# Kernel tuning notes

Measured on AMD Instinct MI355X. Metric: run time of the kernel, lower is better.

Reference implementation:

```python
import jax, jax.numpy as jnp
import numpy as np
import math

MAX_LEN = 65536
NUM_HEADS = 16
HEAD_DIM = 64
K_MAX = 64
LOCAL_WINDOW = 512
LOG_N = math.ceil(math.log2(MAX_LEN + 1))   # 17
LEAF_START = 2 ** LOG_N                      # segment-tree leaf offset


def cover_set(pos):
    """O(log n) segment-tree nodes covering prefix [0..pos-1], each with leaf-depth."""
    if pos <= 0:
        return []
    l, r = LEAF_START, LEAF_START + min(pos, MAX_LEN)
    out = []
    while l < r:
        if l & 1:
            out.append((l, LOG_N - int(math.floor(math.log2(l)))))
            l += 1
        if r & 1:
            r -= 1
            out.append((r, LOG_N - int(math.floor(math.log2(r)))))
        l >>= 1
        r >>= 1
    return out


def node_content(v_tokens, node_idx, depth):
    """Content of a FULL subtree node under the concat/pairwise-mean gated merge.
    Equals: concat tokens while K<=k_max, then (left+right)/2 elementwise, which
    collapses to a strided mean over chunks of size L//K_MAX. Returns (H, K, D)."""
    L = 1 << depth
    a = (node_idx << depth) - LEAF_START          # first token covered by node
    chunk = v_tokens[a:a + L]                     # (L, H, D), static slice
    if L <= K_MAX:
        f = chunk                                 # (L, H, D)
    else:
        f = chunk.reshape(L // K_MAX, K_MAX, NUM_HEADS, HEAD_DIM).mean(0)  # (K_MAX,H,D)
    return jnp.transpose(f, (1, 0, 2))            # (H, K, D)


def setup_inputs() -> dict:
    key = jax.random.key(0)
    k1, k2, k3 = jax.random.split(key, 3)
    v_tokens = jax.random.normal(k1, (50000, NUM_HEADS, HEAD_DIM), jnp.float32)
    q_new = jax.random.normal(k2, (1, NUM_HEADS, HEAD_DIM), jnp.float32)
    depth_proj_w = jax.random.normal(k3, (LOG_N + 1, HEAD_DIM, HEAD_DIM), jnp.float32) * 0.02
    depth_temp = jnp.linspace(0.5, 4.0, LOG_N + 1).astype(jnp.float32)
    return {"v_tokens": v_tokens, "q_new": q_new, "depth_proj_w": depth_proj_w,
            "depth_temp": depth_temp, "n_tokens": 50000}


def reference(v_tokens, q_new, depth_proj_w, depth_temp, n_tokens):
    pos = int(n_tokens)
    q = q_new[0]                                   # (H, D)
    inv_sqrt_d = 1.0 / math.sqrt(HEAD_DIM)

    # --- local window attention over last min(pos, W) tokens (chronological) ---
    n_local = min(pos, LOCAL_WINDOW)
    v_local = v_tokens[pos - n_local:pos]          # (W, H, D)
    s = jnp.einsum('hd,khd->hk', q, v_local) * inv_sqrt_d
    w = jax.nn.softmax(s, axis=-1)
    local_out = jnp.einsum('hk,khd->hd', w, v_local)   # (H, D)

    # --- multi-depth causal tree attention over the O(log n) cover set ---
    node_outs = []
    for node_idx, depth in cover_set(pos):
        f = node_content(v_tokens, node_idx, depth)    # (H, K, D)
        q_depth = q + q @ depth_proj_w[depth].T        # depth-specific query delta
        scale = 1.0 / ((jax.nn.softplus(depth_temp[depth]) + 1e-6) * math.sqrt(HEAD_DIM))
        s = jnp.einsum('hd,hkd->hk', q_depth, f) * scale
        w = jnp.einsum('hk,hkd->hd', jax.nn.softmax(s, axis=-1), f)
        node_outs.append(w)
    if node_outs:
        tree_out = jnp.stack(node_outs, axis=0).mean(0)
    else:
        tree_out = jnp.zeros_like(local_out)

    return (local_out + tree_out)[None]            # (1, H, D)
```

## Files before the change

### kernel.cpp

```cpp
#include <hip/hip_runtime.h>
#include <math.h>

#define NUM_HEADS   16
#define HEAD_DIM    64
#define KMAXN       64
#define LOCAL_WIN   512
#define LOG_N       17
#define LEAF_START  131072
#define MAX_LEN_TOK 65536
#define ROW         1024
#define SLICE       65536
#define MAXN        34

struct K1Args {
    int nNodes;
    int a[MAXN];
    int cpb[MAXN];
    int C[MAXN];
    int CB[MAXN];
    int K[MAXN];
    int off[MAXN];
    int bbase[MAXN];
};

struct K2Args {
    int nNodes;
    int K[MAXN];
    int C[MAXN];
    int CB[MAXN];
    int off[MAXN];
    int depth[MAXN];
};

__device__ __forceinline__ void f4add(float4& a, const float4& b) {
    a.x += b.x; a.y += b.y; a.z += b.z; a.w += b.w;
}

__global__ __launch_bounds__(256) void k1_reduce(const float* __restrict__ v,
                                                 float* __restrict__ ws,
                                                 K1Args A) {
    int b = blockIdx.x;
    int node = 0;
    for (int i = 1; i < A.nNodes; ++i)
        if (b >= A.bbase[i]) node = i;
    int lb  = b - A.bbase[node];
    int CB  = A.CB[node];
    int kg  = lb / CB;
    int cb  = lb - kg * CB;
    int k0  = kg * 16;
    int K   = A.K[node];
    int RK  = K - k0; if (RK > 16) RK = 16;
    int c0  = cb * A.cpb[node];
    int c1  = c0 + A.cpb[node];
    int C   = A.C[node];
    if (c1 > C) c1 = C;

    int j = threadIdx.x;

    float4 acc[16];
    #pragma unroll
    for (int r = 0; r < 16; ++r) acc[r] = make_float4(0.f, 0.f, 0.f, 0.f);

    if (RK == 16) {
        for (int c = c0; c < c1; ++c) {
            const float* p = v + (long)(A.a[node] + c * 64 + k0) * ROW + j * 4;
            float4 x[16];
            #pragma unroll
            for (int r = 0; r < 16; ++r) x[r] = *(const float4*)(p + r * ROW);
            #pragma unroll
            for (int r = 0; r < 16; ++r) f4add(acc[r], x[r]);
        }
    } else {
        for (int c = c0; c < c1; ++c) {
            const float* p = v + (long)(A.a[node] + c * 64 + k0) * ROW + j * 4;
            for (int r = 0; r < RK; ++r) f4add(acc[r], *(const float4*)(p + r * ROW));
        }
    }

    float* wp = ws + (long)A.off[node] + (long)cb * SLICE + (long)k0 * ROW + j * 4;
    for (int r = 0; r < RK; ++r)
        *(float4*)(wp + (long)r * ROW) = acc[r];
}

__global__ __launch_bounds__(256) void k1b_finalize(const float* __restrict__ ws_in,
                                                    float* __restrict__ f,
                                                    K2Args A) {
    int node = blockIdx.y;
    int k    = blockIdx.x;
    if (k >= A.K[node]) return;
    int CB = A.CB[node];
    const float* pf = ws_in + (long)A.off[node] + (long)k * ROW + threadIdx.x * 4;
    float4 a0 = make_float4(0.f,0.f,0.f,0.f);
    float4 a1 = a0, a2 = a0, a3 = a0;
    int cb = 0;
    for (; cb + 4 <= CB; cb += 4) {
        f4add(a0, *(const float4*)(pf + (long)cb * SLICE));
        f4add(a1, *(const float4*)(pf + (long)(cb+1) * SLICE));
        f4add(a2, *(const float4*)(pf + (long)(cb+2) * SLICE));
        f4add(a3, *(const float4*)(pf + (long)(cb+3) * SLICE));
    }
    for (; cb < CB; ++cb) f4add(a0, *(const float4*)(pf + (long)cb * SLICE));
    f4add(a0,a1); f4add(a2,a3); f4add(a0,a2);
    float invC = 1.0f / (float)A.C[node];
    a0.x*=invC; a0.y*=invC; a0.z*=invC; a0.w*=invC;
    *(float4*)(f + ((long)node * 64 + k) * ROW + threadIdx.x * 4) = a0;
}

__global__ __launch_bounds__(256) void k2_node_attn(const float* __restrict__ f,
                                                    const float* __restrict__ q,
                                                    const float* __restrict__ W,
                                                    const float* __restrict__ temp,
                                                    float* __restrict__ node_out,
                                                    K2Args A) {
    int h    = blockIdx.x;
    int node = blockIdx.y;
    int lane = threadIdx.x & 63;
    int w    = threadIdx.x >> 6;
    int K    = A.K[node];
    int dep  = A.depth[node];
    const float* pf = f + (long)node * SLICE + h * 64;

    __shared__ float qs[64], qds[64], sv[64], ps[64];
    __shared__ float red[4][64];

    if (threadIdx.x < 64) qs[lane] = q[h * 64 + lane];
    __syncthreads();

    float qp = 0.f;
    const float* Wr = W + ((long)dep * 64 + lane) * 64;
    #pragma unroll
    for (int e = w * 16; e < w * 16 + 16; ++e) qp += qs[e] * Wr[e];
    red[w][lane] = qp;
    __syncthreads();
    if (w == 0) qds[lane] = qs[lane] + red[0][lane] + red[1][lane] + red[2][lane] + red[3][lane];
    __syncthreads();
    float qd = qds[lane];

    float sp    = log1pf(expf(temp[dep]));
    float scale = 1.0f / ((sp + 1e-6f) * 8.0f);

    for (int k = w; k < K; k += 4) {
        float p = qd * pf[(long)k * ROW + lane];
        #pragma unroll
        for (int m = 1; m < 64; m <<= 1) p += __shfl_xor(p, m, 64);
        if (lane == 0) sv[k] = p * scale;
    }
    __syncthreads();

    if (w == 0) {
        float s  = (lane < K) ? sv[lane] : -1e30f;
        float mx = s;
        #pragma unroll
        for (int m = 1; m < 64; m <<= 1) mx = fmaxf(mx, __shfl_xor(mx, m, 64));
        float e = (lane < K) ? expf(s - mx) : 0.f;
        float S = e;
        #pragma unroll
        for (int m = 1; m < 64; m <<= 1) S += __shfl_xor(S, m, 64);
        ps[lane] = e / S;
    }
    __syncthreads();

    float o = 0.f;
    for (int k = w; k < K; k += 4) o += ps[k] * pf[(long)k * ROW + lane];
    red[w][lane] = o;
    __syncthreads();
    if (w == 0)
        node_out[node * ROW + h * 64 + lane] =
            red[0][lane] + red[1][lane] + red[2][lane] + red[3][lane];
}

__global__ __launch_bounds__(512) void k3_local(const float* __restrict__ v,
                                                const float* __restrict__ q,
                                                const float* __restrict__ node_out,
                                                int nNodes, int pos,
                                                float* __restrict__ out) {
    int h    = blockIdx.x;
    int tid  = threadIdx.x;
    int lane = tid & 63;
    int w    = tid >> 6;
    int nloc = pos < LOCAL_WIN ? pos : LOCAL_WIN;
    int t0   = pos - nloc;

    __shared__ float qs[64];
    __shared__ float sc[LOCAL_WIN];
    __shared__ float red[8][64];
    __shared__ float wred[16];
    __shared__ float mS[2];

    if (tid < 64) qs[tid] = q[h * 64 + tid];
    __syncthreads();

    float s = -1e30f;
    if (tid < nloc) {
        const float* vr = v + (long)(t0 + tid) * ROW + h * 64;
        float acc = 0.f;
        #pragma unroll 8
        for (int d = 0; d < 64; ++d) acc += qs[d] * vr[d];
        s = acc * 0.125f;
    }
    float mx = s;
    #pragma unroll
    for (int m = 1; m < 64; m <<= 1) mx = fmaxf(mx, __shfl_xor(mx, m, 64));
    if (lane == 0) wred[w] = mx;
    __syncthreads();
    if (tid == 0) {
        float m2 = wred[0];
        for (int i = 1; i < 8; ++i) m2 = fmaxf(m2, wred[i]);
        mS[0] = m2;
    }
    __syncthreads();
    float m = mS[0];

    float e = (tid < nloc) ? expf(s - m) : 0.f;
    sc[tid] = e;
    float su = e;
    #pragma unroll
    for (int mm = 1; mm < 64; mm <<= 1) su += __shfl_xor(su, mm, 64);
    if (lane == 0) wred[8 + w] = su;
    __syncthreads();
    if (tid == 0) {
        float S2 = 0.f;
        for (int i = 0; i < 8; ++i) S2 += wred[8 + i];
        mS[1] = S2;
    }
    __syncthreads();
    float S = mS[1];

    float acc = 0.f;
    {
        const float* vb = v + (long)t0 * ROW + h * 64 + lane;
        int tb = w * 64;
        #pragma unroll 4
        for (int i = 0; i < 64; ++i) {
            int t = tb + i;
            if (t < nloc) acc += sc[t] * vb[(long)t * ROW];
        }
    }
    red[w][lane] = acc;
    __syncthreads();

    if (w == 0) {
        float tot = 0.f;
        #pragma unroll
        for (int i = 0; i < 8; ++i) tot += red[i][lane];
        tot = (nloc > 0) ? tot / S : 0.f;
        float tr = 0.f;
        for (int n = 0; n < nNodes; ++n) tr += node_out[n * ROW + h * 64 + lane];
        if (nNodes > 0) tr /= (float)nNodes;
        out[h * 64 + lane] = tot + tr;
    }
}

static int floor_log2_host(unsigned x) { int r = 0; while (x >>= 1) ++r; return r; }

extern "C" void kernel_launch(void* const* d_in, const int* in_sizes, int n_in,
                              void* d_out, int out_size, void* d_ws, size_t ws_size,
                              hipStream_t stream) {
    const float* v    = (const float*)d_in[0];
    const float* q    = (const float*)d_in[1];
    const float* W    = (const float*)d_in[2];
    const float* temp = (const float*)d_in[3];
    float* out        = (float*)d_out;
    float* ws         = (float*)d_ws;

    int pos = in_sizes[0] / ROW;

    int n_nodes = 0;
    int nv[MAXN], nd[MAXN];
    if (pos > 0) {
        long l = LEAF_START;
        long r = LEAF_START + (pos < MAX_LEN_TOK ? pos : MAX_LEN_TOK);
        while (l < r) {
            if (l & 1) { nv[n_nodes] = (int)l; nd[n_nodes] = LOG_N - floor_log2_host((unsigned)l); ++n_nodes; ++l; }
            if (r & 1) { --r; nv[n_nodes] = (int)r; nd[n_nodes] = LOG_N - floor_log2_host((unsigned)r); ++n_nodes; }
            l >>= 1; r >>= 1;
        }
    }

    int cpb_choice = 1024;
    for (int cand : {8, 16, 32, 64, 128, 256, 512, 1024}) {
        long tot_cb = 0;
        for (int i = 0; i < n_nodes; ++i) {
            int L = 1 << nd[i];
            int C = (L > KMAXN) ? L / KMAXN : 1;
            tot_cb += (C + cand - 1) / cand;
        }
        long need = ((tot_cb + n_nodes) * (long)SLICE + (long)n_nodes * ROW) * 4;
        if (need <= (long)ws_size) { cpb_choice = cand; break; }
    }

    K1Args A1{}; K2Args A2{};
    A1.nNodes = n_nodes; A2.nNodes = n_nodes;
    int off = 0, bb = 0;
    for (int i = 0; i < n_nodes; ++i) {
        int depth = nd[i];
        int L = 1 << depth;
        int a = (nv[i] << depth) - LEAF_START;
        int K = (L < KMAXN) ? L : KMAXN;
        int C = (L > KMAXN) ? L / KMAXN : 1;
        int CB = (C + cpb_choice - 1) / cpb_choice;
        int cpb = (C + CB - 1) / CB;
        int kgc = (K + 15) / 16;
        A1.a[i] = a;   A1.cpb[i] = cpb; A1.C[i] = C; A1.CB[i] = CB; A1.K[i] = K;
        A1.off[i] = off; A1.bbase[i] = bb;
        A2.K[i] = K;   A2.C[i] = C;    A2.CB[i] = CB;
        A2.off[i] = off; A2.depth[i] = depth;
        off += CB * SLICE;
        bb  += kgc * CB;
    }
    float* f_buf     = ws + (long)off;
    float* node_outp = f_buf + (long)n_nodes * SLICE;

    if (n_nodes > 0) {
        hipLaunchKernelGGL(k1_reduce, dim3(bb), dim3(256), 0, stream, v, ws, A1);
        hipLaunchKernelGGL(k1b_finalize, dim3(64, n_nodes), dim3(256), 0, stream,
                           ws, f_buf, A2);
        hipLaunchKernelGGL(k2_node_attn, dim3(NUM_HEADS, n_nodes), dim3(256), 0, stream,
                           f_buf, q, W, temp, node_outp, A2);
    }
    hipLaunchKernelGGL(k3_local, dim3(NUM_HEADS), dim3(512), 0, stream,
                       v, q, node_outp, n_nodes, pos, out);
}
```

Measured before the change: 351.5 us.

## Split reduce blocks into 4-row groups with nontemporal loads and occupancy hint

Each k1_reduce block now covers 4 of the K rows instead of 16, so four times as many blocks are launched and each thread holds four accumulators instead of sixteen. The block index order changes so that row groups vary fastest within a chunk range. The inner loop is unrolled over two chunks and reads through nontemporal loads, and launch_bounds asks for 4 blocks per SM. The aim is more parallelism and higher occupancy on this streaming read, at the cost of more blocks and less memory-level parallelism per thread.

```diff
diff --git a/kernel.cpp b/kernel.cpp
--- a/kernel.cpp
+++ b/kernel.cpp
@@ -12,6 +12,12 @@
 #define SLICE       65536
 #define MAXN        34
 
+typedef float vf4 __attribute__((ext_vector_type(4)));
+
+__device__ __forceinline__ vf4 ntload(const float* p) {
+    return __builtin_nontemporal_load((const vf4*)p);
+}
+
 struct K1Args {
     int nNodes;
     int a[MAXN];
@@ -36,50 +42,66 @@
     a.x += b.x; a.y += b.y; a.z += b.z; a.w += b.w;
 }
 
-__global__ __launch_bounds__(256) void k1_reduce(const float* __restrict__ v,
-                                                 float* __restrict__ ws,
-                                                 K1Args A) {
+__global__ __launch_bounds__(256, 4) void k1_reduce(const float* __restrict__ v,
+                                                    float* __restrict__ ws,
+                                                    K1Args A) {
     int b = blockIdx.x;
     int node = 0;
     for (int i = 1; i < A.nNodes; ++i)
         if (b >= A.bbase[i]) node = i;
     int lb  = b - A.bbase[node];
-    int CB  = A.CB[node];
-    int kg  = lb / CB;
-    int cb  = lb - kg * CB;
-    int k0  = kg * 16;
     int K   = A.K[node];
-    int RK  = K - k0; if (RK > 16) RK = 16;
+    int kgc = (K + 3) >> 2;
+    int cb  = lb / kgc;
+    int kg  = lb - cb * kgc;
+    int k0  = kg * 4;
+    int RK  = K - k0; if (RK > 4) RK = 4;
     int c0  = cb * A.cpb[node];
     int c1  = c0 + A.cpb[node];
     int C   = A.C[node];
     if (c1 > C) c1 = C;
 
-    int j = threadIdx.x;
-
-    float4 acc[16];
-    #pragma unroll
-    for (int r = 0; r < 16; ++r) acc[r] = make_float4(0.f, 0.f, 0.f, 0.f);
-
-    if (RK == 16) {
-        for (int c = c0; c < c1; ++c) {
-            const float* p = v + (long)(A.a[node] + c * 64 + k0) * ROW + j * 4;
-            float4 x[16];
-            #pragma unroll
-            for (int r = 0; r < 16; ++r) x[r] = *(const float4*)(p + r * ROW);
-            #pragma unroll
-            for (int r = 0; r < 16; ++r) f4add(acc[r], x[r]);
+    int j4 = threadIdx.x * 4;
+
+    vf4 acc0 = 0.f, acc1 = 0.f, acc2 = 0.f, acc3 = 0.f;
+
+    if (RK == 4) {
+        int c = c0;
+        for (; c + 2 <= c1; c += 2) {
+            const float* p0 = v + (long)(A.a[node] + c * 64 + k0) * ROW + j4;
+            const float* p1 = p0 + SLICE;
+            vf4 y0 = ntload(p0);
+            vf4 y1 = ntload(p0 + ROW);
+            vf4 y2 = ntload(p0 + 2 * ROW);
+            vf4 y3 = ntload(p0 + 3 * ROW);
+            vf4 z0 = ntload(p1);
+            vf4 z1 = ntload(p1 + ROW);
+            vf4 z2 = ntload(p1 + 2 * ROW);
+            vf4 z3 = ntload(p1 + 3 * ROW);
+            acc0 += y0 + z0; acc1 += y1 + z1; acc2 += y2 + z2; acc3 += y3 + z3;
+        }
+        if (c < c1) {
+            const float* p0 = v + (long)(A.a[node] + c * 64 + k0) * ROW + j4;
+            acc0 += ntload(p0);
+            acc1 += ntload(p0 + ROW);
+            acc2 += ntload(p0 + 2 * ROW);
+            acc3 += ntload(p0 + 3 * ROW);
         }
     } else {
         for (int c = c0; c < c1; ++c) {
-            const float* p = v + (long)(A.a[node] + c * 64 + k0) * ROW + j * 4;
-            for (int r = 0; r < RK; ++r) f4add(acc[r], *(const float4*)(p + r * ROW));
-        }
-    }
-
-    float* wp = ws + (long)A.off[node] + (long)cb * SLICE + (long)k0 * ROW + j * 4;
-    for (int r = 0; r < RK; ++r)
-        *(float4*)(wp + (long)r * ROW) = acc[r];
+            const float* p0 = v + (long)(A.a[node] + c * 64 + k0) * ROW + j4;
+            if (RK > 0) acc0 += ntload(p0);
+            if (RK > 1) acc1 += ntload(p0 + ROW);
+            if (RK > 2) acc2 += ntload(p0 + 2 * ROW);
+            if (RK > 3) acc3 += ntload(p0 + 3 * ROW);
+        }
+    }
+
+    float* wp = ws + (long)A.off[node] + (long)cb * SLICE + (long)k0 * ROW + j4;
+    if (RK > 0) *(vf4*)(wp)           = acc0;
+    if (RK > 1) *(vf4*)(wp + ROW)     = acc1;
+    if (RK > 2) *(vf4*)(wp + 2 * ROW) = acc2;
+    if (RK > 3) *(vf4*)(wp + 3 * ROW) = acc3;
 }
 
 __global__ __launch_bounds__(256) void k1b_finalize(const float* __restrict__ ws_in,
@@ -300,7 +322,7 @@
         int C = (L > KMAXN) ? L / KMAXN : 1;
         int CB = (C + cpb_choice - 1) / cpb_choice;
         int cpb = (C + CB - 1) / CB;
-        int kgc = (K + 15) / 16;
+        int kgc = (K + 3) / 4;
         A1.a[i] = a;   A1.cpb[i] = cpb; A1.C[i] = C; A1.CB[i] = CB; A1.K[i] = K;
         A1.off[i] = off; A1.bbase[i] = bb;
         A2.K[i] = K;   A2.C[i] = C;    A2.CB[i] = CB;
```

After: 315.2 us. 10.3% less time.
